# Kernel tuning notes

Measured on AMD Instinct MI355X. Metric: run time of the kernel, lower is better.

Reference implementation:

```python
import jax, jax.numpy as jnp
import numpy as np

B, T, D_MODEL = 2, 1024, 1024
HEAD_DIM = 128
NUM_HEADS = D_MODEL // HEAD_DIM          # 8
EXPAND_V = 1
HEAD_V = HEAD_DIM * EXPAND_V             # 128
KEY_DIM = NUM_HEADS * HEAD_DIM           # 1024
VALUE_DIM = NUM_HEADS * HEAD_V           # 1024
CONV_SIZE = 4
NUM_LEVELS = int(np.log2(T)) + 1         # 11 Fenwick levels
EPS = 1e-5
SCALE = HEAD_DIM ** -0.5


def setup_inputs() -> dict:
    ks = jax.random.split(jax.random.key(0), 20)
    w = lambda i, shp: 0.02 * jax.random.normal(ks[i], shp, jnp.float32)
    return {
        'x': jax.random.normal(ks[0], (B, T, D_MODEL), jnp.float32),
        'cos': jax.random.normal(ks[1], (T, HEAD_DIM), jnp.float32),
        'sin': jax.random.normal(ks[2], (T, HEAD_DIM), jnp.float32),
        'Wq': w(3, (D_MODEL, KEY_DIM)),
        'Wk': w(4, (D_MODEL, KEY_DIM)),
        'Wv': w(5, (D_MODEL, VALUE_DIM)),
        'Wb': w(6, (D_MODEL, NUM_HEADS)),
        'Wa': w(7, (D_MODEL, NUM_HEADS)),
        'Wl': w(8, (D_MODEL, NUM_HEADS * NUM_LEVELS)),
        'Wg': w(9, (D_MODEL, VALUE_DIM)),
        'Wo': w(10, (VALUE_DIM, D_MODEL)),
        'conv_q': 0.2 * jax.random.normal(ks[11], (KEY_DIM, CONV_SIZE), jnp.float32),
        'conv_k': 0.2 * jax.random.normal(ks[12], (KEY_DIM, CONV_SIZE), jnp.float32),
        'conv_v': 0.2 * jax.random.normal(ks[13], (VALUE_DIM, CONV_SIZE), jnp.float32),
        'A_log': jnp.log(jax.random.uniform(ks[14], (NUM_HEADS,), jnp.float32, 1.0, 16.0)),
        'dt_bias': jnp.log(jnp.expm1(jax.random.uniform(ks[15], (NUM_HEADS,), jnp.float32, 0.001, 0.1))),
        'norm_w': jnp.ones((HEAD_V,), jnp.float32),
    }


def _dwconv_silu(x, w):
    # causal depthwise conv1d (ShortConvolution, activation=silu). x:[B,T,C], w:[C,K]
    xp = jnp.pad(x, ((0, 0), (CONV_SIZE - 1, 0), (0, 0)))
    y = jax.lax.conv_general_dilated(xp, w.T[:, None, :], (1,), 'VALID',
                                     dimension_numbers=('NHC', 'HIO', 'NHC'),
                                     feature_group_count=w.shape[0])
    return jax.nn.silu(y)


def _l2norm(x):
    return x * jax.lax.rsqrt(jnp.sum(x * x, -1, keepdims=True) + 1e-6)


def _levels():
    # Fenwick-tree level of token s (0-indexed) in the prefix decomposition at time t:
    # level(t,s) = floor(log2((t+1) XOR s)) for s <= t.
    n = jnp.arange(1, T + 1, dtype=jnp.int32)[:, None]
    s = jnp.arange(T, dtype=jnp.int32)[None, :]
    xval = jnp.maximum(jnp.bitwise_xor(n, s), 1)
    lev = jnp.floor(jnp.log2(xval.astype(jnp.float32))).astype(jnp.int32)
    return jnp.clip(lev, 0, NUM_LEVELS - 1)  # [T,T]


def _forward(x, Wq, Wk, Wv, Wb, Wa, Wl, Wg, Wo, conv_q, conv_k, conv_v, A_log, dt_bias, norm_w):
    # projections + short conv + silu, split heads -> [B,H,T,d]
    q = _dwconv_silu(x @ Wq, conv_q).reshape(B, T, NUM_HEADS, HEAD_DIM).transpose(0, 2, 1, 3)
    k = _dwconv_silu(x @ Wk, conv_k).reshape(B, T, NUM_HEADS, HEAD_DIM).transpose(0, 2, 1, 3)
    v = _dwconv_silu(x @ Wv, conv_v).reshape(B, T, NUM_HEADS, HEAD_V).transpose(0, 2, 1, 3)
    q = _l2norm(q) * SCALE
    k = _l2norm(k)
    beta = jax.nn.sigmoid(x @ Wb).transpose(0, 2, 1)                      # [B,H,T]
    g = -jnp.exp(A_log) * jax.nn.softplus(x @ Wa + dt_bias)              # [B,T,H] log-decay per step
    gc = jnp.cumsum(g.transpose(0, 2, 1), axis=-1)                        # [B,H,T]
    lam = jax.nn.sigmoid(x @ Wl).reshape(B, T, NUM_HEADS, NUM_LEVELS).transpose(0, 2, 1, 3)  # [B,H,T,L]

    idx = jnp.arange(T)
    causal = idx[:, None] >= idx[None, :]
    strict = idx[:, None] > idx[None, :]
    # stable decay matrix D[t,s] = exp(gc_t - gc_s) <= 1 for s <= t
    logD = gc[..., :, None] - gc[..., None, :]
    Dm = jnp.exp(jnp.where(causal, logD, -jnp.inf))                       # [B,H,T,T]

    # WY / UT transform of the gated delta rule:
    #   u_t = beta_t * v_t - beta_t * sum_{s<t} (k_t . k_s) exp(gc_t-gc_s) u_s
    Akk = jnp.einsum('bhtd,bhsd->bhts', k, k) * Dm * strict
    u = jax.scipy.linalg.solve_triangular(beta[..., None] * Akk,
                                          beta[..., None] * v,
                                          lower=True, unit_diagonal=True)  # [B,H,T,dv]

    # log-linear (hierarchical) readout: o_t = sum_s lam_t[level(t,s)] * (q_t.k_s) D[t,s] * u_s
    P = jnp.einsum('bhtd,bhsd->bhts', q, k) * Dm
    M = jnp.take_along_axis(lam, _levels()[None, None], axis=3)           # [B,H,T,T]
    o = jnp.einsum('bhts,bhsd->bhtd', P * M, u).transpose(0, 2, 1, 3)      # [B,T,H,dv]

    # gated RMSNorm output gate, then output projection
    gate = (x @ Wg).reshape(B, T, NUM_HEADS, HEAD_V)
    o = o * jax.lax.rsqrt(jnp.mean(o * o, -1, keepdims=True) + EPS) * norm_w * jax.nn.silu(gate)
    return o.reshape(B, T, VALUE_DIM) @ Wo


def reference(x, cos, sin, Wq, Wk, Wv, Wb, Wa, Wl, Wg, Wo, conv_q, conv_k, conv_v, A_log, dt_bias, norm_w):
    # cos/sin are accepted (block signature) but unused, matching the source module.
    return _forward(x, Wq, Wk, Wv, Wb, Wa, Wl, Wg, Wo, conv_q, conv_k, conv_v, A_log, dt_bias, norm_w)
```

## Files before the change

### kernel.cpp

```cpp
#include <hip/hip_runtime.h>
#include <hip/hip_bf16.h>
#include <math.h>

#define SCALE_Q 0.08838834764831845f

typedef __bf16 bf16x8 __attribute__((ext_vector_type(8)));
typedef float f32x4 __attribute__((ext_vector_type(4)));

static __device__ __forceinline__ float sigm(float x){ return 1.f/(1.f+__expf(-x)); }
static __device__ __forceinline__ ushort f2b(float v){
  __hip_bfloat16 t = __float2bfloat16(v);
  return __builtin_bit_cast(ushort, t);
}
static __device__ __forceinline__ float b2f(ushort u){
  unsigned v = (unsigned)u << 16; return __builtin_bit_cast(float, v);
}

__global__ __launch_bounds__(256) void cast_x(const float* __restrict__ X,
    ushort* __restrict__ Y)
{
  int idx = blockIdx.x*256 + threadIdx.x;
  float4 v = *(const float4*)&X[(size_t)idx*4];
  ushort4 o; o.x=f2b(v.x); o.y=f2b(v.y); o.z=f2b(v.z); o.w=f2b(v.w);
  *(ushort4*)&Y[(size_t)idx*4] = o;
}

__global__ __launch_bounds__(256) void transcast(const float* __restrict__ W,
    ushort* __restrict__ Wt)
{
  __shared__ float tile[32][36];
  int n0 = blockIdx.x*32, k0 = blockIdx.y*32;
  int tid = threadIdx.x;
  int r = tid >> 3, c4 = (tid & 7) << 2;
  *(float4*)&tile[r][c4] = *(const float4*)&W[(size_t)(k0 + r)*1024 + n0 + c4];
  __syncthreads();
  ushort4 o;
  o.x = f2b(tile[c4+0][r]); o.y = f2b(tile[c4+1][r]);
  o.z = f2b(tile[c4+2][r]); o.w = f2b(tile[c4+3][r]);
  *(ushort4*)&Wt[(size_t)(n0 + r)*1024 + k0 + c4] = o;
}

__global__ __launch_bounds__(256) void copy_wsmall(const float* __restrict__ Wb,
    const float* __restrict__ Wa, const float* __restrict__ Wl, float* __restrict__ Wsm)
{
  int idx = blockIdx.x*256 + threadIdx.x;
  if (idx >= 1024*104) return;
  int k = idx / 104, c = idx % 104;
  float v = (c < 8) ? Wb[k*8+c] : (c < 16) ? Wa[k*8+(c-8)] : Wl[k*88+(c-16)];
  Wsm[idx] = v;
}

__global__ __launch_bounds__(256) void gemm_bf16(const ushort* __restrict__ A,
    const ushort* __restrict__ Bt, void* __restrict__ C0, float* __restrict__ C1,
    int M, int N, int K, int nsplit, int ld0, int ld1, int c0bf16)
{
  __shared__ ushort As[2][128*32];
  __shared__ ushort Bs[2][128*32];
  int tid = threadIdx.x;
  int gx = gridDim.x;
  int nwg = gx * gridDim.y;
  int id = blockIdx.y * gx + blockIdx.x;
  int id2 = (id & 7) * (nwg >> 3) + (id >> 3);
  int bm = (id2 / gx) * 128, bn = (id2 % gx) * 128;
  int wave = tid >> 6, lane = tid & 63;
  int wm = (wave >> 1) * 64, wn = (wave & 1) * 64;
  int l16 = lane & 15, kh = lane >> 4;
  f32x4 acc[4][4] = {};
  int rowA0 = tid >> 2, boA = (tid & 3) * 16;
  int niter = K >> 5;

  {
    #pragma unroll
    for (int j = 0; j < 2; ++j) {
      int row = rowA0 + j*64;
      const char* gA = (const char*)A + (((size_t)(bm+row)*K)*2 + boA);
      const char* gB = (const char*)Bt + (((size_t)(bn+row)*K)*2 + boA);
      __builtin_amdgcn_global_load_lds((const __attribute__((address_space(1))) unsigned*)gA,
        (__attribute__((address_space(3))) unsigned*)((char*)&As[0][0] + row*64 + boA), 16, 0, 0);
      __builtin_amdgcn_global_load_lds((const __attribute__((address_space(1))) unsigned*)gB,
        (__attribute__((address_space(3))) unsigned*)((char*)&Bs[0][0] + row*64 + boA), 16, 0, 0);
    }
  }
  __syncthreads();
  int cur = 0;
  for (int i = 0; i < niter; ++i) {
    if (i + 1 < niter) {
      int k0 = (i+1) << 5;
      char* al = (char*)&As[cur^1][0];
      char* bl = (char*)&Bs[cur^1][0];
      #pragma unroll
      for (int j = 0; j < 2; ++j) {
        int row = rowA0 + j*64;
        const char* gA = (const char*)A + (((size_t)(bm+row)*K + k0)*2 + boA);
        const char* gB = (const char*)Bt + (((size_t)(bn+row)*K + k0)*2 + boA);
        __builtin_amdgcn_global_load_lds((const __attribute__((address_space(1))) unsigned*)gA,
          (__attribute__((address_space(3))) unsigned*)(al + row*64 + boA), 16, 0, 0);
        __builtin_amdgcn_global_load_lds((const __attribute__((address_space(1))) unsigned*)gB,
          (__attribute__((address_space(3))) unsigned*)(bl + row*64 + boA), 16, 0, 0);
      }
    }
    bf16x8 af[4], bfr[4];
    #pragma unroll
    for (int ii = 0; ii < 4; ++ii)
      af[ii] = *(bf16x8*)((char*)&As[cur][0] + (wm + ii*16 + l16)*64 + kh*16);
    #pragma unroll
    for (int j = 0; j < 4; ++j)
      bfr[j] = *(bf16x8*)((char*)&Bs[cur][0] + (wn + j*16 + l16)*64 + kh*16);
    #pragma unroll
    for (int ii = 0; ii < 4; ++ii)
      #pragma unroll
      for (int j = 0; j < 4; ++j)
        acc[ii][j] = __builtin_amdgcn_mfma_f32_16x16x32_bf16(af[ii], bfr[j], acc[ii][j], 0, 0, 0);
    __syncthreads();
    cur ^= 1;
  }
  int rg = lane >> 4;
  #pragma unroll
  for (int i = 0; i < 4; ++i) {
    #pragma unroll
    for (int j = 0; j < 4; ++j) {
      int col = bn + wn + j*16 + l16;
      #pragma unroll
      for (int r = 0; r < 4; ++r) {
        int row = bm + wm + i*16 + rg*4 + r;
        float v = acc[i][j][r];
        if (col < nsplit) {
          if (c0bf16) ((ushort*)C0)[(size_t)row*ld0 + col] = f2b(v);
          else        ((float*)C0)[(size_t)row*ld0 + col] = v;
        } else C1[(size_t)row*ld1 + (col - nsplit)] = v;
      }
    }
  }
}

__global__ __launch_bounds__(256) void skinny104(const float* __restrict__ X,
    const float* __restrict__ Wsm, float* __restrict__ part)
{
  __shared__ float XL[64][132];
  __shared__ float WsL[128][112];
  int tid = threadIdx.x;
  int m0 = blockIdx.x << 6;
  int k0 = blockIdx.y << 7;
  #pragma unroll
  for (int j = 0; j < 8; ++j) {
    int s = tid + j*256;
    int row = s >> 5, c4 = (s & 31) << 2;
    *(float4*)&XL[row][c4] = *(const float4*)&X[(size_t)(m0 + row)*1024 + k0 + c4];
  }
  {
    int k = tid >> 1, c = 104 + ((tid & 1) << 2);
    *(float4*)&WsL[k][c] = (float4){0.f,0.f,0.f,0.f};
  }
  {
    int k = tid >> 1, cb = (tid & 1) * 52;
    #pragma unroll
    for (int j = 0; j < 13; ++j) {
      *(float4*)&WsL[k][cb + j*4] = *(const float4*)&Wsm[(size_t)(k0 + k)*104 + cb + j*4];
    }
  }
  __syncthreads();
  int row = tid >> 2, cq = tid & 3;
  int cbase = cq * 28;
  f32x4 acc[7] = {};
  const float* xrow = &XL[row][0];
  #pragma unroll 4
  for (int k = 0; k < 128; ++k) {
    float xv = xrow[k];
    const f32x4* wr = (const f32x4*)&WsL[k][cbase];
    #pragma unroll
    for (int j = 0; j < 7; ++j) acc[j] += xv * wr[j];
  }
  float* pr = &part[((size_t)blockIdx.y*2048 + m0 + row)*104 + cbase];
  int nst = (cq == 3) ? 5 : 7;
  for (int j = 0; j < nst; ++j) *(f32x4*)&pr[j*4] = acc[j];
}

__global__ __launch_bounds__(256) void reduce8(const float* __restrict__ part,
    float* __restrict__ xs)
{
  int idx = blockIdx.x*256 + threadIdx.x;
  float s = 0.f;
  #pragma unroll
  for (int i = 0; i < 8; ++i) s += part[(size_t)i*212992 + idx];
  xs[idx] = s;
}

__global__ __launch_bounds__(256) void conv_silu(const ushort* __restrict__ X,
    const float* __restrict__ W, float* __restrict__ Yf, ushort* __restrict__ Yb,
    int mode, int ldx)
{
  int row = blockIdx.x;
  int b = row >> 10, t = row & 1023;
  int tid = threadIdx.x;
  int c0 = tid << 2;
  float w[4][4];
  #pragma unroll
  for (int c = 0; c < 4; ++c) {
    float4 wv = *(const float4*)&W[(c0 + c)*4];
    w[c][0]=wv.x; w[c][1]=wv.y; w[c][2]=wv.z; w[c][3]=wv.w;
  }
  float acc[4] = {0.f,0.f,0.f,0.f};
  #pragma unroll
  for (int j = 0; j < 4; ++j) {
    int tt = t - 3 + j;
    if (tt >= 0) {
      ushort4 xv = *(const ushort4*)&X[(size_t)(b*1024 + tt)*ldx + c0];
      acc[0] += w[0][j]*b2f(xv.x); acc[1] += w[1][j]*b2f(xv.y);
      acc[2] += w[2][j]*b2f(xv.z); acc[3] += w[3][j]*b2f(xv.w);
    }
  }
  #pragma unroll
  for (int c = 0; c < 4; ++c) acc[c] *= sigm(acc[c]);
  if (mode < 2) {
    float ss = acc[0]*acc[0]+acc[1]*acc[1]+acc[2]*acc[2]+acc[3]*acc[3];
    ss += __shfl_xor(ss, 1); ss += __shfl_xor(ss, 2); ss += __shfl_xor(ss, 4);
    ss += __shfl_xor(ss, 8); ss += __shfl_xor(ss, 16);
    float r = rsqrtf(ss + 1e-6f);
    if (mode == 0) r *= SCALE_Q;
    acc[0]*=r; acc[1]*=r; acc[2]*=r; acc[3]*=r;
  }
  size_t o = (size_t)(b*1024 + t)*1024 + c0;
  if (mode != 0) {
    float4 yv; yv.x=acc[0]; yv.y=acc[1]; yv.z=acc[2]; yv.w=acc[3];
    *(float4*)&Yf[o] = yv;
  }
  if (mode != 2) {
    ushort4 yb; yb.x=f2b(acc[0]); yb.y=f2b(acc[1]); yb.z=f2b(acc[2]); yb.w=f2b(acc[3]);
    *(ushort4*)&Yb[o] = yb;
  }
}

__global__ __launch_bounds__(256) void gc2(const float* __restrict__ xs,
    const float* __restrict__ A_log, const float* __restrict__ dt_bias,
    float* __restrict__ gc)
{
  int bh = blockIdx.x, b = bh >> 3, h = bh & 7;
  __shared__ float sc[256];
  int tid = threadIdx.x;
  float aexp = __expf(A_log[h]), db = dt_bias[h];
  int t0 = tid*4;
  float g[4], csum = 0.f;
  #pragma unroll
  for (int z = 0; z < 4; ++z) {
    float zv = xs[(size_t)(b*1024 + t0 + z)*104 + 8 + h] + db;
    float sp = (zv > 20.f) ? zv : log1pf(__expf(zv));
    csum += -aexp*sp;
    g[z] = csum;
  }
  sc[tid] = csum;
  __syncthreads();
  for (int ofs = 1; ofs < 256; ofs <<= 1) {
    float v = (tid >= ofs) ? sc[tid-ofs] : 0.f;
    __syncthreads();
    sc[tid] += v;
    __syncthreads();
  }
  float excl = sc[tid] - csum;
  #pragma unroll
  for (int z = 0; z < 4; ++z) gc[bh*1024 + t0 + z] = excl + g[z];
}

__global__ __launch_bounds__(256) void chunk_prep(const float* __restrict__ Kg,
    const float* __restrict__ Vg, const float* __restrict__ xs,
    const float* __restrict__ gcg, float* __restrict__ cw, ushort* __restrict__ cWk16,
    ushort* __restrict__ cKpT16, float* __restrict__ eD)
{
  int blk = blockIdx.x;
  int bh = blk >> 4, ck = blk & 15;
  int b = bh >> 3, h = bh & 7;
  int a = ck << 6;
  __shared__ float Kc[64][132];
  __shared__ float As[64][68];
  __shared__ float gcl[65];
  __shared__ float bl[64];
  __shared__ float egc[64];
  __shared__ float edt[64];
  int tid = threadIdx.x;
  for (int e = tid; e < 64*32; e += 256) {
    int t = e >> 5, c4 = (e & 31) << 2;
    *(float4*)&Kc[t][c4] = *(const float4*)&Kg[(size_t)(b*1024 + a + t)*1024 + h*128 + c4];
  }
  if (tid < 64) {
    gcl[tid] = gcg[bh*1024 + a + tid];
    bl[tid] = sigm(xs[(size_t)(b*1024 + a + tid)*104 + h]);
  }
  if (tid == 64) gcl[64] = (ck < 15) ? gcg[bh*1024 + a + 64] : 0.f;
  __syncthreads();
  if (tid < 64) {
    egc[tid] = __expf(gcl[tid] - gcl[0]);
    edt[tid] = (ck < 15) ? __expf(gcl[64] - gcl[tid]) : 0.f;
  }
  {
    int ti = tid >> 4, si = tid & 15;
    if (si <= ti) {
      float dot[4][4] = {};
      for (int kk = 0; kk < 128; kk += 4) {
        float4 kt[4], ks[4];
        #pragma unroll
        for (int z = 0; z < 4; ++z) kt[z] = *(float4*)&Kc[ti*4+z][kk];
        #pragma unroll
        for (int z = 0; z < 4; ++z) ks[z] = *(float4*)&Kc[si*4+z][kk];
        #pragma unroll
        for (int i = 0; i < 4; ++i)
          #pragma unroll
          for (int j = 0; j < 4; ++j)
            dot[i][j] += kt[i].x*ks[j].x + kt[i].y*ks[j].y + kt[i].z*ks[j].z + kt[i].w*ks[j].w;
      }
      #pragma unroll
      for (int i = 0; i < 4; ++i) {
        int t = ti*4 + i;
        #pragma unroll
        for (int j = 0; j < 4; ++j) {
          int s = si*4 + j;
          if (s < t) As[t][s] = bl[t]*dot[i][j]*__expf(gcl[t]-gcl[s]);
        }
      }
    }
  }
  __syncthreads();
  int c = tid;
  float u[64];
  if (c < 128) {
    #pragma unroll
    for (int t = 0; t < 64; ++t)
      u[t] = bl[t]*Vg[(size_t)(b*1024 + a + t)*1024 + h*128 + c];
  } else {
    int d = c - 128;
    #pragma unroll
    for (int t = 0; t < 64; ++t)
      u[t] = bl[t]*egc[t]*Kc[t][d];
  }
  #pragma unroll
  for (int t = 1; t < 64; ++t) {
    float acc = u[t];
    int s = 0;
    #pragma unroll
    for (; s + 4 <= t; s += 4) {
      float4 a4 = *(float4*)&As[t][s];
      acc -= a4.x*u[s] + a4.y*u[s+1] + a4.z*u[s+2] + a4.w*u[s+3];
    }
    #pragma unroll
    for (; s < t; ++s) acc -= As[t][s]*u[s];
    u[t] = acc;
  }
  size_t cbase = (size_t)blk*8192;
  if (c < 128) {
    #pragma unroll
    for (int t = 0; t < 64; ++t)
      cw[cbase + t*128 + c] = u[t];
  } else {
    int d = c - 128;
    #pragma unroll
    for (int t = 0; t < 64; ++t) {
      cWk16[cbase + t*128 + d] = f2b(-u[t]);
      cKpT16[cbase + d*64 + t] = f2b(Kc[t][d]*edt[t]);
    }
  }
  if (tid == 0) eD[blk] = (ck < 15) ? __expf(gcl[64]-gcl[0]) : 0.f;
}

__global__ __launch_bounds__(256) void chunk_scan6(const float* __restrict__ cw,
    const ushort* __restrict__ cWk16, const ushort* __restrict__ cKpT16,
    const float* __restrict__ eD, ushort* __restrict__ Ut)
{
  int blk = blockIdx.x;
  int slice = blk >> 4, bh = blk & 15;
  int e_base = slice << 3;
  __shared__ ushort Wks[2][8192];
  __shared__ ushort Kps[2][8192];
  __shared__ ushort StT[16*128];
  __shared__ ushort usT[16*64];
  __shared__ float  Stf[128*16];
  int tid = threadIdx.x;
  int wave = tid >> 6, lane = tid & 63;
  int l15 = lane & 15, kh = lane >> 4;
  for (int idx = tid; idx < 16*128; idx += 256) StT[idx] = 0;
  for (int idx = tid; idx < 16*64; idx += 256) usT[idx] = 0;
  for (int idx = tid; idx < 128*16; idx += 256) Stf[idx] = 0.f;

  int e = l15;
  int t0 = wave*16 + kh*4;
  int ci0 = bh << 4;
  f32x4 wcur = {0.f,0.f,0.f,0.f};
  if (e < 8) {
    #pragma unroll
    for (int r = 0; r < 4; ++r)
      wcur[r] = cw[(size_t)ci0*8192 + (t0+r)*128 + e_base + e];
  }
  {
    const char* wg = (const char*)(cWk16 + (size_t)ci0*8192);
    const char* kg = (const char*)(cKpT16 + (size_t)ci0*8192);
    #pragma unroll
    for (int j = 0; j < 4; ++j) {
      unsigned off = (j<<12) + (tid<<4);
      unsigned wrow = off >> 8, wslot = (off >> 4) & 15;
      unsigned wsrc = wrow*256 + ((wslot ^ (wrow & 15)) << 4);
      __builtin_amdgcn_global_load_lds((const __attribute__((address_space(1))) unsigned*)(wg + wsrc),
        (__attribute__((address_space(3))) unsigned*)((char*)&Wks[0][0] + off), 16, 0, 0);
      unsigned krow = off >> 7, kslot = (off >> 4) & 7;
      unsigned ksrc = krow*128 + ((kslot ^ (krow & 7)) << 4);
      __builtin_amdgcn_global_load_lds((const __attribute__((address_space(1))) unsigned*)(kg + ksrc),
        (__attribute__((address_space(3))) unsigned*)((char*)&Kps[0][0] + off), 16, 0, 0);
    }
  }
  __syncthreads();

  for (int i = 0; i < 16; ++i) {
    int ci = ci0 + i, a = i << 6, cur = i & 1;
    f32x4 wnext = {0.f,0.f,0.f,0.f};
    if (i < 15) {
      if (e < 8) {
        #pragma unroll
        for (int r = 0; r < 4; ++r)
          wnext[r] = cw[(size_t)(ci+1)*8192 + (t0+r)*128 + e_base + e];
      }
      const char* wg = (const char*)(cWk16 + (size_t)(ci+1)*8192);
      const char* kg = (const char*)(cKpT16 + (size_t)(ci+1)*8192);
      char* wl = (char*)&Wks[cur^1][0];
      char* kl = (char*)&Kps[cur^1][0];
      #pragma unroll
      for (int j = 0; j < 4; ++j) {
        unsigned off = (j<<12) + (tid<<4);
        unsigned wrow = off >> 8, wslot = (off >> 4) & 15;
        unsigned wsrc = wrow*256 + ((wslot ^ (wrow & 15)) << 4);
        __builtin_amdgcn_global_load_lds((const __attribute__((address_space(1))) unsigned*)(wg + wsrc),
          (__attribute__((address_space(3))) unsigned*)(wl + off), 16, 0, 0);
        unsigned krow = off >> 7, kslot = (off >> 4) & 7;
        unsigned ksrc = krow*128 + ((kslot ^ (krow & 7)) << 4);
        __builtin_amdgcn_global_load_lds((const __attribute__((address_space(1))) unsigned*)(kg + ksrc),
          (__attribute__((address_space(3))) unsigned*)(kl + off), 16, 0, 0);
      }
    }
    {
      f32x4 d = wcur;
      const char* wkb = (const char*)&Wks[cur][0];
      int arow = wave*16 + l15;
      #pragma unroll
      for (int ks = 0; ks < 4; ++ks) {
        bf16x8 afr = *(const bf16x8*)(wkb + arow*256 + (((ks*4 + kh) ^ l15) << 4));
        bf16x8 bfr = *(const bf16x8*)((const char*)StT + l15*256 + (((ks*4 + kh) ^ l15) << 4));
        d = __builtin_amdgcn_mfma_f32_16x16x32_bf16(afr, bfr, d, 0, 0, 0);
      }
      if (e < 8) {
        ushort4 uw;
        uw.x = f2b(d[0]); uw.y = f2b(d[1]); uw.z = f2b(d[2]); uw.w = f2b(d[3]);
        *(ushort4*)((char*)usT + e*128 + (((t0>>3) ^ (e&7)) << 4) + (t0&7)*2) = uw;
        *(ushort4*)&Ut[(size_t)(bh*128 + e_base + e)*1024 + a + t0] = uw;
      }
    }
    asm volatile("s_waitcnt lgkmcnt(0)" ::: "memory");
    __builtin_amdgcn_s_barrier();
    __builtin_amdgcn_sched_barrier(0);
    if (i < 15) {
      float ed = eD[ci];
      const char* kpb = (const char*)&Kps[cur][0];
      #pragma unroll
      for (int mt = 0; mt < 2; ++mt) {
        int krow = (wave*2 + mt)*16 + l15;
        int k0 = (wave*2 + mt)*16 + kh*4;
        f32x4 c;
        #pragma unroll
        for (int r = 0; r < 4; ++r) c[r] = ed * Stf[(k0+r)*16 + e];
        #pragma unroll
        for (int ts = 0; ts < 2; ++ts) {
          bf16x8 afr = *(const bf16x8*)(kpb + krow*128 + (((ts*4 + kh) ^ (krow&7)) << 4));
          bf16x8 bfr = *(const bf16x8*)((const char*)usT + l15*128 + (((ts*4 + kh) ^ (l15&7)) << 4));
          c = __builtin_amdgcn_mfma_f32_16x16x32_bf16(afr, bfr, c, 0, 0, 0);
        }
        #pragma unroll
        for (int r = 0; r < 4; ++r) Stf[(k0+r)*16 + e] = c[r];
        if (e < 8) {
          ushort4 sw;
          sw.x = f2b(c[0]); sw.y = f2b(c[1]); sw.z = f2b(c[2]); sw.w = f2b(c[3]);
          *(ushort4*)((char*)StT + e*256 + (((k0>>3) ^ e) << 4) + (k0&7)*2) = sw;
        }
      }
      wcur = wnext;
      asm volatile("s_waitcnt vmcnt(0) lgkmcnt(0)" ::: "memory");
      __builtin_amdgcn_s_barrier();
      __builtin_amdgcn_sched_barrier(0);
    }
  }
}

__global__ __launch_bounds__(256) void readout3(const ushort* __restrict__ Qb,
    const ushort* __restrict__ Kb, const ushort* __restrict__ Ut,
    const float* __restrict__ gcg, const float* __restrict__ xs,
    float* __restrict__ Og)
{
  int blk = blockIdx.x;
  int bh = blk >> 4, ic = blk & 15;
  int half = blockIdx.y;
  int b = bh >> 3, h = bh & 7;
  int tbase = ic << 6;
  __shared__ ushort Ks[2][8192];
  __shared__ ushort Us[2][8192];
  __shared__ ushort Pl[4][1024];
  __shared__ float lamS[64][12];
  int tid = threadIdx.x;
  int wave = tid >> 6, lane = tid & 63;
  int l15 = lane & 15, kh = lane >> 4;

  const char* kgb = (const char*)Kb + ((size_t)(b*1024)*1024 + h*128)*2;
  const char* ugb = (const char*)Ut + ((size_t)(bh*128)*1024)*2;

  for (int e = tid; e < 64*11; e += 256) {
    int t = e/11, l = e%11;
    lamS[t][l] = sigm(xs[(size_t)(b*1024+tbase+t)*104 + 16 + h*11 + l]);
  }
  int tl = kh*4;
  float gct_r[4];
  #pragma unroll
  for (int r = 0; r < 4; ++r) gct_r[r] = gcg[bh*1024 + tbase + wave*16 + tl + r];
  bf16x8 qf[4];
  {
    const ushort* qp = &Qb[(size_t)(b*1024 + tbase + wave*16 + l15)*1024 + h*128 + kh*8];
    #pragma unroll
    for (int kk = 0; kk < 4; ++kk) qf[kk] = *(const bf16x8*)(qp + kk*32);
  }

  f32x4 accO[8] = {};
  int nsteps = ic + 1;
  int jmid = (nsteps + 1) >> 1;
  int j0 = half ? jmid : 0;
  int j1 = half ? nsteps : jmid;
  ushort* Pw = &Pl[wave][0];

  if (j0 < j1) {
    {
      const char* kg = kgb + (size_t)(j0<<6)*2048;
      const char* ug = ugb + (size_t)(j0<<6)*2;
      #pragma unroll
      for (int it = 0; it < 4; ++it) {
        unsigned off = (it<<12) + (tid<<4);
        unsigned krow = off >> 8, kc = (off >> 4) & 15;
        unsigned ksrc = krow*2048 + ((kc ^ (krow & 15)) << 4);
        __builtin_amdgcn_global_load_lds((const __attribute__((address_space(1))) unsigned*)(kg + ksrc),
          (__attribute__((address_space(3))) unsigned*)((char*)&Ks[0][0] + off), 16, 0, 0);
        unsigned ud = off >> 7, uc = (off >> 4) & 7;
        unsigned usrc = ud*2048 + ((uc ^ (ud & 7)) << 4);
        __builtin_amdgcn_global_load_lds((const __attribute__((address_space(1))) unsigned*)(ug + usrc),
          (__attribute__((address_space(3))) unsigned*)((char*)&Us[0][0] + off), 16, 0, 0);
      }
    }
    __syncthreads();
    int cur = 0;
    for (int j = j0; j < j1; ++j) {
      int sbase = j << 6;
      if (j + 1 < j1) {
        const char* kg = kgb + (size_t)((j+1)<<6)*2048;
        const char* ug = ugb + (size_t)((j+1)<<6)*2;
        char* kl = (char*)&Ks[cur^1][0];
        char* ul = (char*)&Us[cur^1][0];
        #pragma unroll
        for (int it = 0; it < 4; ++it) {
          unsigned off = (it<<12) + (tid<<4);
          unsigned krow = off >> 8, kc = (off >> 4) & 15;
          unsigned ksrc = krow*2048 + ((kc ^ (krow & 15)) << 4);
          __builtin_amdgcn_global_load_lds((const __attribute__((address_space(1))) unsigned*)(kg + ksrc),
            (__attribute__((address_space(3))) unsigned*)(kl + off), 16, 0, 0);
          unsigned ud = off >> 7, uc = (off >> 4) & 7;
          unsigned usrc = ud*2048 + ((uc ^ (ud & 7)) << 4);
          __builtin_amdgcn_global_load_lds((const __attribute__((address_space(1))) unsigned*)(ug + usrc),
            (__attribute__((address_space(3))) unsigned*)(ul + off), 16, 0, 0);
        }
      }
      float gcs_r[4];
      #pragma unroll
      for (int jt = 0; jt < 4; ++jt)
        gcs_r[jt] = gcg[bh*1024 + sbase + jt*16 + l15];
      f32x4 accS[4] = {};
      const char* ksb = (const char*)&Ks[cur][0];
      #pragma unroll
      for (int jt = 0; jt < 4; ++jt) {
        int row = jt*16 + l15;
        int rsw = row & 15;
        #pragma unroll
        for (int kk = 0; kk < 4; ++kk) {
          bf16x8 kf = *(const bf16x8*)(ksb + row*256 + (((kk*4 + kh) ^ rsw) << 4));
          accS[jt] = __builtin_amdgcn_mfma_f32_16x16x32_bf16(qf[kk], kf, accS[jt], 0, 0, 0);
        }
      }
      #pragma unroll
      for (int jt = 0; jt < 4; ++jt) {
        int sg = sbase + jt*16 + l15;
        #pragma unroll
        for (int r = 0; r < 4; ++r) {
          int t_loc = tl + r;
          int tg = tbase + wave*16 + t_loc;
          float pv = 0.f;
          if (sg <= tg) {
            int lev = 31 - __clz((unsigned)((tg+1) ^ sg));
            lev = lev > 10 ? 10 : lev;
            pv = accS[jt][r] * __expf(gct_r[r] - gcs_r[jt]) * lamS[wave*16 + t_loc][lev];
          }
          int bo = (t_loc << 7) + ((jt*16 + l15) << 1);
          bo ^= (t_loc & 7) << 4;
          *(ushort*)((char*)Pw + bo) = f2b(pv);
        }
      }
      const char* usb = (const char*)&Us[cur][0];
      #pragma unroll
      for (int ks = 0; ks < 2; ++ks) {
        int bo = (l15 << 7) + ((ks*32 + kh*8) << 1);
        bo ^= (l15 & 7) << 4;
        bf16x8 pa = *(bf16x8*)((char*)Pw + bo);
        #pragma unroll
        for (int dt = 0; dt < 8; ++dt) {
          int d = dt*16 + l15;
          bf16x8 uf = *(const bf16x8*)(usb + d*128 + (((ks*4 + kh) ^ (d & 7)) << 4));
          accO[dt] = __builtin_amdgcn_mfma_f32_16x16x32_bf16(pa, uf, accO[dt], 0, 0, 0);
        }
      }
      __syncthreads();
      cur ^= 1;
    }
  }
  float* og = Og + (size_t)half*2097152;
  #pragma unroll
  for (int dt = 0; dt < 8; ++dt) {
    #pragma unroll
    for (int r = 0; r < 4; ++r) {
      int row = tbase + wave*16 + tl + r;
      og[(size_t)(b*1024 + row)*1024 + h*128 + dt*16 + l15] = accO[dt][r];
    }
  }
}

__global__ __launch_bounds__(64) void normgate(const float* __restrict__ O1,
    const float* __restrict__ O2, const float* __restrict__ G,
    const float* __restrict__ norm_w, ushort* __restrict__ Y)
{
  int row = blockIdx.x;
  int lane = threadIdx.x;
  size_t base = (size_t)(row >> 3)*1024 + (size_t)(row & 7)*128;
  float2 oa = *(const float2*)&O1[base + lane*2];
  float2 ob = *(const float2*)&O2[base + lane*2];
  float ox = oa.x + ob.x, oy = oa.y + ob.y;
  float ss = ox*ox + oy*oy;
  #pragma unroll
  for (int m = 1; m < 64; m <<= 1) ss += __shfl_xor(ss, m);
  float r = rsqrtf(ss * (1.f/128.f) + 1e-5f);
  float2 g = *(const float2*)&G[base + lane*2];
  ushort2 y;
  y.x = f2b(ox * r * norm_w[lane*2+0] * (g.x * sigm(g.x)));
  y.y = f2b(oy * r * norm_w[lane*2+1] * (g.y * sigm(g.y)));
  *(ushort2*)&Y[base + lane*2] = y;
}

extern "C" void kernel_launch(void* const* d_in, const int* in_sizes, int n_in,
                              void* d_out, int out_size, void* d_ws, size_t ws_size,
                              hipStream_t stream)
{
  const float* x    = (const float*)d_in[0];
  const float* Wq   = (const float*)d_in[3];
  const float* Wk   = (const float*)d_in[4];
  const float* Wv   = (const float*)d_in[5];
  const float* Wb   = (const float*)d_in[6];
  const float* Wa   = (const float*)d_in[7];
  const float* Wl   = (const float*)d_in[8];
  const float* Wg   = (const float*)d_in[9];
  const float* Wo   = (const float*)d_in[10];
  const float* cq   = (const float*)d_in[11];
  const float* ck   = (const float*)d_in[12];
  const float* cv   = (const float*)d_in[13];
  const float* A_log   = (const float*)d_in[14];
  const float* dt_bias = (const float*)d_in[15];
  const float* norm_w  = (const float*)d_in[16];
  float* out = (float*)d_out;

  float* p = (float*)d_ws;
  float* xqkv = p;  p += 6291456;
  float* xg   = p;  p += 2097152;
  float* kb   = p;  p += 2097152;
  float* vb   = p;  p += 2097152;
  float* o1   = p;  p += 2097152;
  float* o2   = p;  p += 2097152;
  float* xs   = p;  p += 212992;
  float* gc   = p;  p += 16384;
  float* eD   = p;  p += 256;
  ushort* x16 = (ushort*)p; p += 1048576;
  ushort* Wt4 = (ushort*)p; p += 2097152;
  ushort* Wot = (ushort*)p; p += 524288;
  float* Wsm  = p;  p += 106496;
  ushort* yb16= (ushort*)p; p += 1048576;
  ushort* qb16= (ushort*)p; p += 1048576;
  ushort* kb16= (ushort*)p; p += 1048576;
  ushort* ut16= (ushort*)p; p += 1048576;
  ushort* xqkv16 = (ushort*)xqkv;
  float* cw  = xqkv;
  ushort* cWk16  = (ushort*)(xqkv + 2097152);
  ushort* cKpT16 = (ushort*)(xqkv + 3145728);
  float* part = o1;

  dim3 blk(256);
  cast_x<<<dim3(2048), blk, 0, stream>>>(x, x16);
  transcast<<<dim3(32,32), blk, 0, stream>>>(Wq, Wt4);
  transcast<<<dim3(32,32), blk, 0, stream>>>(Wk, Wt4 + 1024*1024);
  transcast<<<dim3(32,32), blk, 0, stream>>>(Wv, Wt4 + 2*1024*1024);
  transcast<<<dim3(32,32), blk, 0, stream>>>(Wg, Wt4 + 3*1024*1024);
  transcast<<<dim3(32,32), blk, 0, stream>>>(Wo, Wot);
  copy_wsmall<<<dim3(416), blk, 0, stream>>>(Wb, Wa, Wl, Wsm);
  gemm_bf16<<<dim3(32,16), blk, 0, stream>>>(x16, Wt4, xqkv16, xg, 2048, 4096, 1024,
                                             3072, 3072, 1024, 1);
  skinny104<<<dim3(32,8), blk, 0, stream>>>(x, Wsm, part);
  reduce8<<<dim3(833), blk, 0, stream>>>(part, xs);
  conv_silu<<<dim3(2048), blk, 0, stream>>>(xqkv16 + 0,    cq, nullptr, qb16, 0, 3072);
  conv_silu<<<dim3(2048), blk, 0, stream>>>(xqkv16 + 1024, ck, kb, kb16, 1, 3072);
  conv_silu<<<dim3(2048), blk, 0, stream>>>(xqkv16 + 2048, cv, vb, nullptr, 2, 3072);
  gc2<<<dim3(16), blk, 0, stream>>>(xs, A_log, dt_bias, gc);
  chunk_prep<<<dim3(256), blk, 0, stream>>>(kb, vb, xs, gc, cw, cWk16, cKpT16, eD);
  chunk_scan6<<<dim3(256), blk, 0, stream>>>(cw, cWk16, cKpT16, eD, ut16);
  readout3<<<dim3(256,2), blk, 0, stream>>>(qb16, kb16, ut16, gc, xs, o1);
  normgate<<<dim3(16384), dim3(64), 0, stream>>>(o1, o2, xg, norm_w, yb16);
  gemm_bf16<<<dim3(8,16), blk, 0, stream>>>(yb16, Wot, out, out, 2048, 1024, 1024,
                                            1024, 1024, 1024, 0);
}
```

Measured before the change: 212.2 us.

## Batch transpose-casts and conv launches into single grids; split GEMM barriers

Merges the five weight transpose-cast launches into one 3D grid and the three depthwise conv+SiLU launches into one 2D grid, selecting pointers by block index. This removes several kernel launches and their tail and launch gaps. Separately, the GEMM main loop replaces __syncthreads with explicit lgkmcnt/vmcnt waits, raw s_barrier and sched_barrier, and skips the barrier on the last iteration. The extra barrier adds one synchronisation per iteration and limits compiler scheduling across it.

```diff
diff --git a/kernel.cpp b/kernel.cpp
--- a/kernel.cpp
+++ b/kernel.cpp
@@ -25,10 +25,15 @@
   *(ushort4*)&Y[(size_t)idx*4] = o;
 }
 
-__global__ __launch_bounds__(256) void transcast(const float* __restrict__ W,
-    ushort* __restrict__ Wt)
+__global__ __launch_bounds__(256) void transcast_all(const float* __restrict__ Wq,
+    const float* __restrict__ Wk, const float* __restrict__ Wv,
+    const float* __restrict__ Wg, const float* __restrict__ Wo,
+    ushort* __restrict__ Wt4, ushort* __restrict__ Wot)
 {
   __shared__ float tile[32][36];
+  int z = blockIdx.z;
+  const float* W = (z==0)?Wq:(z==1)?Wk:(z==2)?Wv:(z==3)?Wg:Wo;
+  ushort* Wt = (z<4)? (Wt4 + (size_t)z*1048576) : Wot;
   int n0 = blockIdx.x*32, k0 = blockIdx.y*32;
   int tid = threadIdx.x;
   int r = tid >> 3, c4 = (tid & 7) << 2;
@@ -81,7 +86,9 @@
         (__attribute__((address_space(3))) unsigned*)((char*)&Bs[0][0] + row*64 + boA), 16, 0, 0);
     }
   }
-  __syncthreads();
+  asm volatile("s_waitcnt vmcnt(0)" ::: "memory");
+  __builtin_amdgcn_s_barrier();
+  __builtin_amdgcn_sched_barrier(0);
   int cur = 0;
   for (int i = 0; i < niter; ++i) {
     if (i + 1 < niter) {
@@ -111,7 +118,14 @@
       #pragma unroll
       for (int j = 0; j < 4; ++j)
         acc[ii][j] = __builtin_amdgcn_mfma_f32_16x16x32_bf16(af[ii], bfr[j], acc[ii][j], 0, 0, 0);
-    __syncthreads();
+    if (i + 1 < niter) {
+      asm volatile("s_waitcnt lgkmcnt(0)" ::: "memory");
+      __builtin_amdgcn_s_barrier();
+      __builtin_amdgcn_sched_barrier(0);
+      asm volatile("s_waitcnt vmcnt(0)" ::: "memory");
+      __builtin_amdgcn_s_barrier();
+      __builtin_amdgcn_sched_barrier(0);
+    }
     cur ^= 1;
   }
   int rg = lane >> 4;
@@ -185,10 +199,14 @@
   xs[idx] = s;
 }
 
-__global__ __launch_bounds__(256) void conv_silu(const ushort* __restrict__ X,
-    const float* __restrict__ W, float* __restrict__ Yf, ushort* __restrict__ Yb,
-    int mode, int ldx)
-{
+__global__ __launch_bounds__(256) void conv_fused(const ushort* __restrict__ Xall,
+    const float* __restrict__ Wq, const float* __restrict__ Wk, const float* __restrict__ Wv,
+    float* __restrict__ kbf, float* __restrict__ vbf,
+    ushort* __restrict__ qb16, ushort* __restrict__ kb16, int ldx)
+{
+  int mode = blockIdx.y;
+  const float* W = (mode==0)?Wq:(mode==1)?Wk:Wv;
+  const ushort* X = Xall + mode*1024;
   int row = blockIdx.x;
   int b = row >> 10, t = row & 1023;
   int tid = threadIdx.x;
@@ -220,13 +238,19 @@
     acc[0]*=r; acc[1]*=r; acc[2]*=r; acc[3]*=r;
   }
   size_t o = (size_t)(b*1024 + t)*1024 + c0;
-  if (mode != 0) {
+  if (mode == 1) {
     float4 yv; yv.x=acc[0]; yv.y=acc[1]; yv.z=acc[2]; yv.w=acc[3];
-    *(float4*)&Yf[o] = yv;
-  }
-  if (mode != 2) {
+    *(float4*)&kbf[o] = yv;
+  } else if (mode == 2) {
+    float4 yv; yv.x=acc[0]; yv.y=acc[1]; yv.z=acc[2]; yv.w=acc[3];
+    *(float4*)&vbf[o] = yv;
+  }
+  if (mode == 0) {
     ushort4 yb; yb.x=f2b(acc[0]); yb.y=f2b(acc[1]); yb.z=f2b(acc[2]); yb.w=f2b(acc[3]);
-    *(ushort4*)&Yb[o] = yb;
+    *(ushort4*)&qb16[o] = yb;
+  } else if (mode == 1) {
+    ushort4 yb; yb.x=f2b(acc[0]); yb.y=f2b(acc[1]); yb.z=f2b(acc[2]); yb.w=f2b(acc[3]);
+    *(ushort4*)&kb16[o] = yb;
   }
 }
 
@@ -695,19 +719,13 @@
 
   dim3 blk(256);
   cast_x<<<dim3(2048), blk, 0, stream>>>(x, x16);
-  transcast<<<dim3(32,32), blk, 0, stream>>>(Wq, Wt4);
-  transcast<<<dim3(32,32), blk, 0, stream>>>(Wk, Wt4 + 1024*1024);
-  transcast<<<dim3(32,32), blk, 0, stream>>>(Wv, Wt4 + 2*1024*1024);
-  transcast<<<dim3(32,32), blk, 0, stream>>>(Wg, Wt4 + 3*1024*1024);
-  transcast<<<dim3(32,32), blk, 0, stream>>>(Wo, Wot);
+  transcast_all<<<dim3(32,32,5), blk, 0, stream>>>(Wq, Wk, Wv, Wg, Wo, Wt4, Wot);
   copy_wsmall<<<dim3(416), blk, 0, stream>>>(Wb, Wa, Wl, Wsm);
   gemm_bf16<<<dim3(32,16), blk, 0, stream>>>(x16, Wt4, xqkv16, xg, 2048, 4096, 1024,
                                              3072, 3072, 1024, 1);
   skinny104<<<dim3(32,8), blk, 0, stream>>>(x, Wsm, part);
   reduce8<<<dim3(833), blk, 0, stream>>>(part, xs);
-  conv_silu<<<dim3(2048), blk, 0, stream>>>(xqkv16 + 0,    cq, nullptr, qb16, 0, 3072);
-  conv_silu<<<dim3(2048), blk, 0, stream>>>(xqkv16 + 1024, ck, kb, kb16, 1, 3072);
-  conv_silu<<<dim3(2048), blk, 0, stream>>>(xqkv16 + 2048, cv, vb, nullptr, 2, 3072);
+  conv_fused<<<dim3(2048,3), blk, 0, stream>>>(xqkv16, cq, ck, cv, kb, vb, qb16, kb16, 3072);
   gc2<<<dim3(16), blk, 0, stream>>>(xs, A_log, dt_bias, gc);
   chunk_prep<<<dim3(256), blk, 0, stream>>>(kb, vb, xs, gc, cw, cWk16, cKpT16, eD);
   chunk_scan6<<<dim3(256), blk, 0, stream>>>(cw, cWk16, cKpT16, eD, ut16);
```

Result: faster. 201.1 us (-5.3%).
